# Kernel optimization log

Hardware: AMD Instinct MI355X
Metric: run time of the kernel (lower is better)

## Reference

```python
import jax, jax.numpy as jnp
import numpy as np

H, DQ, DK, DV, DM = 16, 64, 64, 64, 1024
NEG = -1.0e12


def setup_inputs() -> dict:
    key = jax.random.key(0)
    ks = jax.random.split(key, 16)
    B, S = 4, 1024
    s = 0.02
    inp = {
        "query": jax.random.normal(ks[0], (B, S, DM), jnp.float32),
        "key": jax.random.normal(ks[1], (B, S, DM), jnp.float32),
        "value": jax.random.normal(ks[2], (B, S, DM), jnp.float32),
        "mask": jax.random.randint(ks[3], (B, S), 0, 2, jnp.int32),
        "Wq": jax.random.normal(ks[4], (H * DQ, DM), jnp.float32) * s,
        "bq": jnp.zeros((H * DQ,), jnp.float32),
        "Wk": jax.random.normal(ks[5], (H * DK, DM), jnp.float32) * s,
        "bk": jnp.zeros((H * DK,), jnp.float32),
        "Wv": jax.random.normal(ks[6], (H * DV, DM), jnp.float32) * s,
        "bv": jnp.zeros((H * DV,), jnp.float32),
        "Wo": jax.random.normal(ks[7], (DM, H * DV), jnp.float32) * s,
        "bo": jnp.zeros((DM,), jnp.float32),
        "ln_g": jnp.ones((DM,), jnp.float32),
        "ln_b": jnp.zeros((DM,), jnp.float32),
    }
    return inp


def _attention(query, key, value, mask, Wq, bq, Wk, bk, Wv, bv, Wo, bo, ln_g, ln_b):
    B, qL, _ = query.shape
    kL = key.shape[1]
    mf = mask.astype(jnp.float32)  # [B, kL] ; 1 = masked token
    # padding mask broadcast over query rows, then self-attn: masked query rows fully masked
    m = jnp.broadcast_to(mf[:, None, :], (B, qL, kL))
    m = jnp.where(mf[:, :, None] > 0, 1.0, m)  # [B, q, k]

    def proj(x, W, b, d):
        # [B,S,DM] -> [H,B,S,d]
        return (x @ W.T + b).reshape(B, -1, H, d).transpose(2, 0, 1, 3)

    q = proj(query, Wq, bq, DQ)
    k = proj(key, Wk, bk, DK)
    v = proj(value, Wv, bv, DV)

    scores = jnp.einsum("hbqd,hbkd->hbqk", q, k) / np.float32(np.sqrt(DK))
    fut = jnp.triu(jnp.ones((qL, kL), jnp.float32), k=1)  # [q,k] future mask
    scores = scores + m[None] * NEG + fut[None, None] * NEG
    attn = jax.nn.softmax(scores, axis=-1)
    attn = attn * (1.0 - m[None]) * (1.0 - fut[None, None])

    out = jnp.einsum("hbqk,hbkd->hbqd", attn, v)  # [H,B,q,DV]
    out = out.transpose(1, 2, 0, 3).reshape(B, qL, H * DV)
    out = out @ Wo.T + bo + query  # residual
    mu = jnp.mean(out, axis=-1, keepdims=True)
    var = jnp.mean(jnp.square(out - mu), axis=-1, keepdims=True)
    out = (out - mu) * jax.lax.rsqrt(var + 1e-12) * ln_g + ln_b
    return out, attn.reshape(H * B, qL, kL)


def reference(query, key, value, mask, Wq, bq, Wk, bk, Wv, bv, Wo, bo, ln_g, ln_b):
    return _attention(query, key, value, mask, Wq, bq, Wk, bk, Wv, bv, Wo, bo, ln_g, ln_b)
```

## Files before the change

kernel.cpp:

```cpp
#include <hip/hip_runtime.h>
#include <hip/hip_bf16.h>

typedef __attribute__((ext_vector_type(4))) float f32x4;
typedef __attribute__((ext_vector_type(4))) float fv4;
typedef __attribute__((ext_vector_type(8))) short bf16x8;
typedef __attribute__((ext_vector_type(4))) short bf16x4;

#define DEVI __device__ __forceinline__

constexpr int BATCH = 4, SEQ = 1024, NH = 16, HD = 64, DM_ = 1024;
constexpr int NTOK = BATCH * SEQ;

DEVI unsigned short f2bf(float f) {
  union { float f; unsigned u; } v; v.f = f;
  unsigned r = v.u + 0x7FFFu + ((v.u >> 16) & 1u);
  return (unsigned short)(r >> 16);
}

DEVI int swz64(int row, int col) {
  int byte = (row * 64 + col) * 2;
  byte ^= (row & 7) << 4;
  return byte >> 1;
}

DEVI void gld_lds16(const unsigned short* g, unsigned short* l) {
  __builtin_amdgcn_global_load_lds(
      (const __attribute__((address_space(1))) unsigned int*)g,
      (__attribute__((address_space(3))) unsigned int*)l, 16, 0, 0);
}

__global__ __launch_bounds__(256) void k_cvt(
    const float* __restrict__ q, const float* __restrict__ k,
    const float* __restrict__ v,
    const float* __restrict__ wq, const float* __restrict__ wk,
    const float* __restrict__ wv, const float* __restrict__ wo,
    unsigned short* __restrict__ Xb, unsigned short* __restrict__ Wb)
{
  const int a = blockIdx.y;
  const float* src;
  unsigned short* dst;
  int n;
  if (a < 3) {
    src = (a == 0) ? q : (a == 1) ? k : v;
    dst = Xb + (size_t)a * NTOK * DM_;
    n = NTOK * DM_;
  } else {
    src = (a == 3) ? wq : (a == 4) ? wk : (a == 5) ? wv : wo;
    dst = Wb + (size_t)(a - 3) * DM_ * DM_;
    n = DM_ * DM_;
  }
  const int idx = (blockIdx.x * 256 + threadIdx.x) * 8;
  if (idx >= n) return;
  fv4 v0 = *(const fv4*)(src + idx);
  fv4 v1 = *(const fv4*)(src + idx + 4);
  bf16x8 o;
  o[0] = (short)f2bf(v0[0]); o[1] = (short)f2bf(v0[1]);
  o[2] = (short)f2bf(v0[2]); o[3] = (short)f2bf(v0[3]);
  o[4] = (short)f2bf(v1[0]); o[5] = (short)f2bf(v1[1]);
  o[6] = (short)f2bf(v1[2]); o[7] = (short)f2bf(v1[3]);
  *(bf16x8*)(dst + idx) = o;
}

__global__ __launch_bounds__(256) void k_proj(
    const unsigned short* __restrict__ Xb, const unsigned short* __restrict__ Wb,
    const float* __restrict__ bq, const float* __restrict__ bk,
    const float* __restrict__ bv,
    unsigned short* __restrict__ qo, unsigned short* __restrict__ ko,
    unsigned short* __restrict__ vTo)
{
  const int z = blockIdx.z;
  const unsigned short* X = Xb + (size_t)z * NTOK * DM_;
  const unsigned short* W = Wb + (size_t)z * DM_ * DM_;
  const float* bias = (z == 0) ? bq : (z == 1) ? bk : bv;

  __shared__ __align__(16) unsigned short Al[64 * 64];
  __shared__ __align__(16) unsigned short Bl[128 * 64];

  const int tid = threadIdx.x;
  const int lane = tid & 63;
  const int w = tid >> 6;
  const int wm = w & 1, wn = w >> 1;
  const int l15 = lane & 15, lg = lane >> 4;
  const int m0 = blockIdx.x * 64;
  const int o0 = blockIdx.y * 128;

  const int rseg = lane >> 3;
  const int cg = (lane & 7) ^ rseg;

  f32x4 acc[2][4];
#pragma unroll
  for (int i = 0; i < 2; ++i)
#pragma unroll
    for (int j = 0; j < 4; ++j) acc[i][j] = f32x4{0.f, 0.f, 0.f, 0.f};

  for (int kt = 0; kt < 16; ++kt) {
    const int k0 = kt * 64;
    __syncthreads();
#pragma unroll
    for (int i = 0; i < 2; ++i) {
      const int seg = w * 2 + i;
      gld_lds16(X + (size_t)(m0 + seg * 8 + rseg) * DM_ + k0 + cg * 8, &Al[seg * 512]);
    }
#pragma unroll
    for (int i = 0; i < 4; ++i) {
      const int seg = w * 4 + i;
      gld_lds16(W + (size_t)(o0 + seg * 8 + rseg) * DM_ + k0 + cg * 8, &Bl[seg * 512]);
    }
    __syncthreads();
#pragma unroll
    for (int kk = 0; kk < 2; ++kk) {
      bf16x8 af[2], bfm[4];
#pragma unroll
      for (int m = 0; m < 2; ++m)
        af[m] = *(const bf16x8*)&Al[swz64(wm * 32 + m * 16 + l15, kk * 32 + lg * 8)];
#pragma unroll
      for (int n = 0; n < 4; ++n)
        bfm[n] = *(const bf16x8*)&Bl[swz64(wn * 64 + n * 16 + l15, kk * 32 + lg * 8)];
#pragma unroll
      for (int m = 0; m < 2; ++m)
#pragma unroll
        for (int n = 0; n < 4; ++n)
          acc[m][n] = __builtin_amdgcn_mfma_f32_16x16x32_bf16(af[m], bfm[n], acc[m][n], 0, 0, 0);
    }
  }

#pragma unroll
  for (int n = 0; n < 4; ++n) {
    const int oc = o0 + wn * 64 + n * 16 + l15;
    const float bb = bias[oc];
#pragma unroll
    for (int m = 0; m < 2; ++m) {
      const int rbase = m0 + wm * 32 + m * 16 + lg * 4;
      if (z == 2) {
        bf16x4 pv;
#pragma unroll
        for (int j = 0; j < 4; ++j) pv[j] = (short)f2bf(acc[m][n][j] + bb);
        *(bf16x4*)&vTo[((size_t)(rbase >> 10) * 1024 + oc) * 1024 + (rbase & 1023)] = pv;
      } else {
        unsigned short* Y = (z == 0) ? qo : ko;
        const float sc = (z == 0) ? 0.125f : 1.f;
#pragma unroll
        for (int j = 0; j < 4; ++j)
          Y[(size_t)(rbase + j) * DM_ + oc] = f2bf((acc[m][n][j] + bb) * sc);
      }
    }
  }
}

__global__ __launch_bounds__(256) void k_attn_pv(
    const unsigned short* __restrict__ qb, const unsigned short* __restrict__ kb,
    const unsigned short* __restrict__ vT, const int* __restrict__ mask,
    float* __restrict__ attn, unsigned short* __restrict__ Ob)
{
  const int tid = threadIdx.x;
  const int lane = tid & 63;
  const int w = tid >> 6;
  const int l15 = lane & 15, lg = lane >> 4;
  const int hb = blockIdx.y;
  const int h = hb >> 2, b = hb & 3;
  const int t = blockIdx.x;
  const int q0 = t * 16;
  const int qglob = q0 + l15;

  __shared__ float Ow[4][64 * 18];
  __shared__ float red[4][16];
  __shared__ float ssum[16];

  const unsigned short* qp = qb + (size_t)(b * SEQ + qglob) * DM_ + h * HD + lg * 8;
  const bf16x8 qf0 = *(const bf16x8*)qp;
  const bf16x8 qf1 = *(const bf16x8*)(qp + 32);

  const int qm = mask[b * SEQ + qglob];
  const int ni = (t >= w) ? (((t - w) >> 2) + 1) : 0;

  f32x4 acc[16];
#pragma unroll
  for (int i = 0; i < 16; ++i) acc[i] = f32x4{0.f, 0.f, 0.f, 0.f};

#pragma unroll
  for (int i = 0; i < 16; ++i) {
    if (i < ni) {
      const int krow = (w + 4 * i) * 16 + l15;
      const unsigned short* kp = kb + (size_t)(b * SEQ + krow) * DM_ + h * HD + lg * 8;
      bf16x8 kf0 = *(const bf16x8*)kp;
      bf16x8 kf1 = *(const bf16x8*)(kp + 32);
      acc[i] = __builtin_amdgcn_mfma_f32_16x16x32_bf16(kf0, qf0, acc[i], 0, 0, 0);
      acc[i] = __builtin_amdgcn_mfma_f32_16x16x32_bf16(kf1, qf1, acc[i], 0, 0, 0);
    }
  }

  unsigned long long kv = 0;
#pragma unroll
  for (int i = 0; i < 16; ++i) {
    if (i < ni) {
      const int kbase = (w + 4 * i) * 16 + lg * 4;
      int4 mv = *(const int4*)&mask[b * SEQ + kbase];
      if (mv.x == 0) kv |= 1ull << (i * 4 + 0);
      if (mv.y == 0) kv |= 1ull << (i * 4 + 1);
      if (mv.z == 0) kv |= 1ull << (i * 4 + 2);
      if (mv.w == 0) kv |= 1ull << (i * 4 + 3);
    }
  }
  if (qm != 0) kv = 0;

  float m = -1e30f;
#pragma unroll
  for (int i = 0; i < 16; ++i) {
    if (i < ni) {
      const int kbase = (w + 4 * i) * 16 + lg * 4;
#pragma unroll
      for (int j = 0; j < 4; ++j)
        if (((kv >> (i * 4 + j)) & 1ull) && (kbase + j <= qglob))
          m = fmaxf(m, acc[i][j]);
    }
  }
  m = fmaxf(m, __shfl_xor(m, 16, 64));
  m = fmaxf(m, __shfl_xor(m, 32, 64));
  if (lane < 16) red[w][l15] = m;
  __syncthreads();
  m = fmaxf(fmaxf(red[0][l15], red[1][l15]), fmaxf(red[2][l15], red[3][l15]));
  __syncthreads();

  float s = 0.f;
#pragma unroll
  for (int i = 0; i < 16; ++i) {
    if (i < ni) {
      const int kbase = (w + 4 * i) * 16 + lg * 4;
#pragma unroll
      for (int j = 0; j < 4; ++j) {
        const bool vld = ((kv >> (i * 4 + j)) & 1ull) && (kbase + j <= qglob);
        const float p = vld ? __expf(acc[i][j] - m) : 0.f;
        acc[i][j] = p;
        s += p;
      }
    }
  }
  s += __shfl_xor(s, 16, 64);
  s += __shfl_xor(s, 32, 64);
  if (lane < 16) red[w][l15] = s;
  __syncthreads();
  s = red[0][l15] + red[1][l15] + red[2][l15] + red[3][l15];
  if (w == 0 && lane < 16) ssum[l15] = s;
  const float rinv = (s > 0.f) ? (1.f / s) : 0.f;

  float* ap = attn + (size_t)hb * SEQ * SEQ + (size_t)qglob * SEQ;
#pragma unroll
  for (int i = 0; i < 16; ++i) {
    const int kbase = (w + 4 * i) * 16 + lg * 4;
    fv4 st = fv4{0.f, 0.f, 0.f, 0.f};
    if (i < ni) {
#pragma unroll
      for (int j = 0; j < 4; ++j) st[j] = acc[i][j] * rinv;
    }
    *(fv4*)&ap[kbase] = st;
  }

  f32x4 o[4];
#pragma unroll
  for (int dt = 0; dt < 4; ++dt) o[dt] = f32x4{0.f, 0.f, 0.f, 0.f};
  const int nc = (ni + 1) >> 1;
  const unsigned short* vbase = vT + (size_t)(b * 1024 + h * HD) * 1024;
#pragma unroll
  for (int c = 0; c < 8; ++c) {
    if (c < nc) {
      const bool hasB = (2 * c + 1 < ni);
      bf16x8 pb;
#pragma unroll
      for (int j = 0; j < 4; ++j) pb[j] = (short)f2bf(acc[2 * c][j]);
#pragma unroll
      for (int j = 0; j < 4; ++j)
        pb[4 + j] = hasB ? (short)f2bf(acc[2 * c + 1][j]) : (short)0;
      const int kA = (w + 8 * c) * 16 + lg * 4;
      const int kB = hasB ? kA + 64 : kA;
#pragma unroll
      for (int dt = 0; dt < 4; ++dt) {
        const unsigned short* vr = vbase + (size_t)(dt * 16 + l15) * 1024;
        bf16x4 a0 = *(const bf16x4*)(vr + kA);
        bf16x4 a1 = *(const bf16x4*)(vr + kB);
        bf16x8 af;
        af[0] = a0[0]; af[1] = a0[1]; af[2] = a0[2]; af[3] = a0[3];
        af[4] = a1[0]; af[5] = a1[1]; af[6] = a1[2]; af[7] = a1[3];
        o[dt] = __builtin_amdgcn_mfma_f32_16x16x32_bf16(af, pb, o[dt], 0, 0, 0);
      }
    }
  }

#pragma unroll
  for (int dt = 0; dt < 4; ++dt)
#pragma unroll
    for (int j = 0; j < 4; ++j)
      Ow[w][(dt * 16 + lg * 4 + j) * 18 + l15] = o[dt][j];
  __syncthreads();

  const int qr = tid >> 4;
  const int d0 = (tid & 15) * 4;
  const float sq = ssum[qr];
  const float ri = (sq > 0.f) ? (1.f / sq) : 0.f;
  bf16x4 ob;
#pragma unroll
  for (int j = 0; j < 4; ++j) {
    const int d = d0 + j;
    const float v = Ow[0][d * 18 + qr] + Ow[1][d * 18 + qr] +
                    Ow[2][d * 18 + qr] + Ow[3][d * 18 + qr];
    ob[j] = (short)f2bf(v * ri);
  }
  *(bf16x4*)&Ob[(size_t)(b * SEQ + q0 + qr) * DM_ + h * HD + d0] = ob;
}

__global__ __launch_bounds__(256) void k_oproj(
    const unsigned short* __restrict__ Ob, const unsigned short* __restrict__ Wb,
    const float* __restrict__ bo, const float* __restrict__ query,
    float* __restrict__ preln)
{
  const unsigned short* W = Wb + (size_t)3 * DM_ * DM_;

  __shared__ __align__(16) unsigned short Al[64 * 64];
  __shared__ __align__(16) unsigned short Bl[128 * 64];

  const int tid = threadIdx.x;
  const int lane = tid & 63;
  const int w = tid >> 6;
  const int wm = w & 1, wn = w >> 1;
  const int l15 = lane & 15, lg = lane >> 4;
  const int m0 = blockIdx.x * 64;
  const int o0 = blockIdx.y * 128;

  const int rseg = lane >> 3;
  const int cg = (lane & 7) ^ rseg;

  f32x4 acc[2][4];
#pragma unroll
  for (int i = 0; i < 2; ++i)
#pragma unroll
    for (int j = 0; j < 4; ++j) acc[i][j] = f32x4{0.f, 0.f, 0.f, 0.f};

  for (int kt = 0; kt < 16; ++kt) {
    const int k0 = kt * 64;
    __syncthreads();
#pragma unroll
    for (int i = 0; i < 2; ++i) {
      const int seg = w * 2 + i;
      gld_lds16(Ob + (size_t)(m0 + seg * 8 + rseg) * DM_ + k0 + cg * 8, &Al[seg * 512]);
    }
#pragma unroll
    for (int i = 0; i < 4; ++i) {
      const int seg = w * 4 + i;
      gld_lds16(W + (size_t)(o0 + seg * 8 + rseg) * DM_ + k0 + cg * 8, &Bl[seg * 512]);
    }
    __syncthreads();
#pragma unroll
    for (int kk = 0; kk < 2; ++kk) {
      bf16x8 af[2], bfm[4];
#pragma unroll
      for (int m = 0; m < 2; ++m)
        af[m] = *(const bf16x8*)&Al[swz64(wm * 32 + m * 16 + l15, kk * 32 + lg * 8)];
#pragma unroll
      for (int n = 0; n < 4; ++n)
        bfm[n] = *(const bf16x8*)&Bl[swz64(wn * 64 + n * 16 + l15, kk * 32 + lg * 8)];
#pragma unroll
      for (int m = 0; m < 2; ++m)
#pragma unroll
        for (int n = 0; n < 4; ++n)
          acc[m][n] = __builtin_amdgcn_mfma_f32_16x16x32_bf16(af[m], bfm[n], acc[m][n], 0, 0, 0);
    }
  }

#pragma unroll
  for (int n = 0; n < 4; ++n) {
    const int oc = o0 + wn * 64 + n * 16 + l15;
    const float bb = bo[oc];
#pragma unroll
    for (int m = 0; m < 2; ++m) {
      const int rbase = m0 + wm * 32 + m * 16 + lg * 4;
#pragma unroll
      for (int j = 0; j < 4; ++j) {
        const size_t idx = (size_t)(rbase + j) * DM_ + oc;
        preln[idx] = acc[m][n][j] + bb + query[idx];
      }
    }
  }
}

__global__ __launch_bounds__(256) void k_ln(
    const float* __restrict__ x, const float* __restrict__ g,
    const float* __restrict__ bta, float* __restrict__ out)
{
  const int row = blockIdx.x;
  const int tid = threadIdx.x;
  const float* xr = x + (size_t)row * DM_;
  fv4 v = *(const fv4*)(xr + tid * 4);
  float s = v[0] + v[1] + v[2] + v[3];
  float s2 = v[0] * v[0] + v[1] * v[1] + v[2] * v[2] + v[3] * v[3];
#pragma unroll
  for (int off = 1; off < 64; off <<= 1) {
    s += __shfl_xor(s, off, 64);
    s2 += __shfl_xor(s2, off, 64);
  }
  __shared__ float rs[2][4];
  const int w = tid >> 6;
  if ((tid & 63) == 0) { rs[0][w] = s; rs[1][w] = s2; }
  __syncthreads();
  s = rs[0][0] + rs[0][1] + rs[0][2] + rs[0][3];
  s2 = rs[1][0] + rs[1][1] + rs[1][2] + rs[1][3];
  const float mu = s * (1.f / 1024.f);
  const float var = s2 * (1.f / 1024.f) - mu * mu;
  const float rstd = rsqrtf(var + 1e-12f);
  fv4 gg = *(const fv4*)(g + tid * 4);
  fv4 bb = *(const fv4*)(bta + tid * 4);
  fv4 o;
#pragma unroll
  for (int j = 0; j < 4; ++j) o[j] = (v[j] - mu) * rstd * gg[j] + bb[j];
  *(fv4*)(out + (size_t)row * DM_ + tid * 4) = o;
}

extern "C" void kernel_launch(void* const* d_in, const int* in_sizes, int n_in,
                              void* d_out, int out_size, void* d_ws, size_t ws_size,
                              hipStream_t stream) {
  const float* query = (const float*)d_in[0];
  const float* key   = (const float*)d_in[1];
  const float* value = (const float*)d_in[2];
  const int*   mask  = (const int*)d_in[3];
  const float* Wq = (const float*)d_in[4];
  const float* bq = (const float*)d_in[5];
  const float* Wk = (const float*)d_in[6];
  const float* bk = (const float*)d_in[7];
  const float* Wv = (const float*)d_in[8];
  const float* bv = (const float*)d_in[9];
  const float* Wo = (const float*)d_in[10];
  const float* bo = (const float*)d_in[11];
  const float* ln_g = (const float*)d_in[12];
  const float* ln_b = (const float*)d_in[13];

  float* out  = (float*)d_out;
  float* attn = out + (size_t)NTOK * DM_;

  char* ws = (char*)d_ws;
  unsigned short* Xb = (unsigned short*)ws;
  unsigned short* Wb = Xb + (size_t)3 * NTOK * DM_;
  unsigned short* qb = Wb + (size_t)4 * DM_ * DM_;
  unsigned short* kb = qb + (size_t)NTOK * DM_;
  unsigned short* vT = kb + (size_t)NTOK * DM_;
  unsigned short* Ob = vT + (size_t)NTOK * DM_;
  float* preln = (float*)ws;

  k_cvt<<<dim3(2048, 7), 256, 0, stream>>>(query, key, value, Wq, Wk, Wv, Wo,
                                           Xb, Wb);
  k_proj<<<dim3(64, 8, 3), 256, 0, stream>>>(Xb, Wb, bq, bk, bv, qb, kb, vT);
  k_attn_pv<<<dim3(64, 64), 256, 0, stream>>>(qb, kb, vT, mask, attn, Ob);
  k_oproj<<<dim3(64, 8), 256, 0, stream>>>(Ob, Wb, bo, query, preln);
  k_ln<<<4096, 256, 0, stream>>>(preln, ln_g, ln_b, out);
}
```

Baseline: 557.3 us.

## Double-buffer projection GEMMs and restructure attention to 32-query blocks with LDS P tile

The q/k/v and output projection GEMMs switch to two LDS buffers, so the next k-tile's global-to-LDS load is issued while MFMAs run on the current tile. This drops one barrier per iteration in exchange for twice the shared memory. The attention kernel now uses 512-thread blocks covering 32 queries, so each K fragment is reused across two query groups. Probabilities are staged in a swizzled LDS tile, so the PV product reads contiguous V rows split across two k-halves. The larger LDS footprint (64KB for P) and higher register use may reduce occupancy.

```diff
diff --git a/kernel.cpp b/kernel.cpp
--- a/kernel.cpp
+++ b/kernel.cpp
@@ -73,8 +73,8 @@
   const unsigned short* W = Wb + (size_t)z * DM_ * DM_;
   const float* bias = (z == 0) ? bq : (z == 1) ? bk : bv;
 
-  __shared__ __align__(16) unsigned short Al[64 * 64];
-  __shared__ __align__(16) unsigned short Bl[128 * 64];
+  __shared__ __align__(16) unsigned short Al[2][64 * 64];
+  __shared__ __align__(16) unsigned short Bl[2][128 * 64];
 
   const int tid = threadIdx.x;
   const int lane = tid & 63;
@@ -93,35 +93,43 @@
 #pragma unroll
     for (int j = 0; j < 4; ++j) acc[i][j] = f32x4{0.f, 0.f, 0.f, 0.f};
 
+#define PROJ_STAGE(nb, kt)                                                     \
+  {                                                                            \
+    const int k0_ = (kt) * 64;                                                 \
+    _Pragma("unroll") for (int i = 0; i < 2; ++i) {                            \
+      const int seg = w * 2 + i;                                               \
+      gld_lds16(X + (size_t)(m0 + seg * 8 + rseg) * DM_ + k0_ + cg * 8,        \
+                &Al[nb][seg * 512]);                                           \
+    }                                                                          \
+    _Pragma("unroll") for (int i = 0; i < 4; ++i) {                            \
+      const int seg = w * 4 + i;                                               \
+      gld_lds16(W + (size_t)(o0 + seg * 8 + rseg) * DM_ + k0_ + cg * 8,        \
+                &Bl[nb][seg * 512]);                                           \
+    }                                                                          \
+  }
+
+  PROJ_STAGE(0, 0);
+  __syncthreads();
+
   for (int kt = 0; kt < 16; ++kt) {
-    const int k0 = kt * 64;
-    __syncthreads();
-#pragma unroll
-    for (int i = 0; i < 2; ++i) {
-      const int seg = w * 2 + i;
-      gld_lds16(X + (size_t)(m0 + seg * 8 + rseg) * DM_ + k0 + cg * 8, &Al[seg * 512]);
-    }
-#pragma unroll
-    for (int i = 0; i < 4; ++i) {
-      const int seg = w * 4 + i;
-      gld_lds16(W + (size_t)(o0 + seg * 8 + rseg) * DM_ + k0 + cg * 8, &Bl[seg * 512]);
-    }
-    __syncthreads();
+    const int cur = kt & 1;
+    if (kt < 15) PROJ_STAGE(cur ^ 1, kt + 1);
 #pragma unroll
     for (int kk = 0; kk < 2; ++kk) {
       bf16x8 af[2], bfm[4];
 #pragma unroll
       for (int m = 0; m < 2; ++m)
-        af[m] = *(const bf16x8*)&Al[swz64(wm * 32 + m * 16 + l15, kk * 32 + lg * 8)];
+        af[m] = *(const bf16x8*)&Al[cur][swz64(wm * 32 + m * 16 + l15, kk * 32 + lg * 8)];
 #pragma unroll
       for (int n = 0; n < 4; ++n)
-        bfm[n] = *(const bf16x8*)&Bl[swz64(wn * 64 + n * 16 + l15, kk * 32 + lg * 8)];
+        bfm[n] = *(const bf16x8*)&Bl[cur][swz64(wn * 64 + n * 16 + l15, kk * 32 + lg * 8)];
 #pragma unroll
       for (int m = 0; m < 2; ++m)
 #pragma unroll
         for (int n = 0; n < 4; ++n)
           acc[m][n] = __builtin_amdgcn_mfma_f32_16x16x32_bf16(af[m], bfm[n], acc[m][n], 0, 0, 0);
     }
+    __syncthreads();
   }
 
 #pragma unroll
@@ -147,7 +155,7 @@
   }
 }
 
-__global__ __launch_bounds__(256) void k_attn_pv(
+__global__ __launch_bounds__(512, 2) void k_attn_pv(
     const unsigned short* __restrict__ qb, const unsigned short* __restrict__ kb,
     const unsigned short* __restrict__ vT, const int* __restrict__ mask,
     float* __restrict__ attn, unsigned short* __restrict__ Ob)
@@ -158,153 +166,207 @@
   const int l15 = lane & 15, lg = lane >> 4;
   const int hb = blockIdx.y;
   const int h = hb >> 2, b = hb & 3;
-  const int t = blockIdx.x;
-  const int q0 = t * 16;
-  const int qglob = q0 + l15;
-
-  __shared__ float Ow[4][64 * 18];
-  __shared__ float red[4][16];
-  __shared__ float ssum[16];
-
-  const unsigned short* qp = qb + (size_t)(b * SEQ + qglob) * DM_ + h * HD + lg * 8;
-  const bf16x8 qf0 = *(const bf16x8*)qp;
-  const bf16x8 qf1 = *(const bf16x8*)(qp + 32);
-
-  const int qm = mask[b * SEQ + qglob];
-  const int ni = (t >= w) ? (((t - w) >> 2) + 1) : 0;
-
-  f32x4 acc[16];
-#pragma unroll
-  for (int i = 0; i < 16; ++i) acc[i] = f32x4{0.f, 0.f, 0.f, 0.f};
-
-#pragma unroll
-  for (int i = 0; i < 16; ++i) {
+  const int bx = blockIdx.x;
+  const int q0 = bx * 32;
+
+  __shared__ __align__(16) unsigned short Pl[32 * 1024];
+  __shared__ float red[8][2][16];
+  __shared__ float ssum[32];
+
+  int qglob[2];
+  qglob[0] = q0 + l15;
+  qglob[1] = q0 + 16 + l15;
+
+  bf16x8 qf[2][2];
+#pragma unroll
+  for (int g = 0; g < 2; ++g) {
+    const unsigned short* qp = qb + (size_t)(b * SEQ + qglob[g]) * DM_ + h * HD + lg * 8;
+    qf[g][0] = *(const bf16x8*)qp;
+    qf[g][1] = *(const bf16x8*)(qp + 32);
+  }
+  int qm[2];
+  qm[0] = mask[b * SEQ + qglob[0]];
+  qm[1] = mask[b * SEQ + qglob[1]];
+
+  const int tt = 2 * bx + 1;
+  const int ni = (tt >= w) ? ((tt - w) >> 3) + 1 : 0;
+
+  bf16x8 kf[8][2];
+#pragma unroll
+  for (int i = 0; i < 8; ++i) {
     if (i < ni) {
-      const int krow = (w + 4 * i) * 16 + l15;
+      const int krow = (w + 8 * i) * 16 + l15;
       const unsigned short* kp = kb + (size_t)(b * SEQ + krow) * DM_ + h * HD + lg * 8;
-      bf16x8 kf0 = *(const bf16x8*)kp;
-      bf16x8 kf1 = *(const bf16x8*)(kp + 32);
-      acc[i] = __builtin_amdgcn_mfma_f32_16x16x32_bf16(kf0, qf0, acc[i], 0, 0, 0);
-      acc[i] = __builtin_amdgcn_mfma_f32_16x16x32_bf16(kf1, qf1, acc[i], 0, 0, 0);
-    }
-  }
-
-  unsigned long long kv = 0;
-#pragma unroll
-  for (int i = 0; i < 16; ++i) {
+      kf[i][0] = *(const bf16x8*)kp;
+      kf[i][1] = *(const bf16x8*)(kp + 32);
+    }
+  }
+
+  f32x4 acc[8][2];
+#pragma unroll
+  for (int i = 0; i < 8; ++i)
+#pragma unroll
+    for (int g = 0; g < 2; ++g) acc[i][g] = f32x4{0.f, 0.f, 0.f, 0.f};
+
+#pragma unroll
+  for (int i = 0; i < 8; ++i) {
     if (i < ni) {
-      const int kbase = (w + 4 * i) * 16 + lg * 4;
+#pragma unroll
+      for (int g = 0; g < 2; ++g) {
+        acc[i][g] = __builtin_amdgcn_mfma_f32_16x16x32_bf16(kf[i][0], qf[g][0], acc[i][g], 0, 0, 0);
+        acc[i][g] = __builtin_amdgcn_mfma_f32_16x16x32_bf16(kf[i][1], qf[g][1], acc[i][g], 0, 0, 0);
+      }
+    }
+  }
+
+  unsigned kvb = 0;
+#pragma unroll
+  for (int i = 0; i < 8; ++i) {
+    if (i < ni) {
+      const int kbase = (w + 8 * i) * 16 + lg * 4;
       int4 mv = *(const int4*)&mask[b * SEQ + kbase];
-      if (mv.x == 0) kv |= 1ull << (i * 4 + 0);
-      if (mv.y == 0) kv |= 1ull << (i * 4 + 1);
-      if (mv.z == 0) kv |= 1ull << (i * 4 + 2);
-      if (mv.w == 0) kv |= 1ull << (i * 4 + 3);
-    }
-  }
-  if (qm != 0) kv = 0;
-
-  float m = -1e30f;
-#pragma unroll
-  for (int i = 0; i < 16; ++i) {
+      if (mv.x == 0) kvb |= 1u << (i * 4 + 0);
+      if (mv.y == 0) kvb |= 1u << (i * 4 + 1);
+      if (mv.z == 0) kvb |= 1u << (i * 4 + 2);
+      if (mv.w == 0) kvb |= 1u << (i * 4 + 3);
+    }
+  }
+
+  float m[2] = {-1e30f, -1e30f};
+#pragma unroll
+  for (int i = 0; i < 8; ++i) {
     if (i < ni) {
-      const int kbase = (w + 4 * i) * 16 + lg * 4;
-#pragma unroll
-      for (int j = 0; j < 4; ++j)
-        if (((kv >> (i * 4 + j)) & 1ull) && (kbase + j <= qglob))
-          m = fmaxf(m, acc[i][j]);
-    }
-  }
-  m = fmaxf(m, __shfl_xor(m, 16, 64));
-  m = fmaxf(m, __shfl_xor(m, 32, 64));
-  if (lane < 16) red[w][l15] = m;
-  __syncthreads();
-  m = fmaxf(fmaxf(red[0][l15], red[1][l15]), fmaxf(red[2][l15], red[3][l15]));
-  __syncthreads();
-
-  float s = 0.f;
-#pragma unroll
-  for (int i = 0; i < 16; ++i) {
+      const int kbase = (w + 8 * i) * 16 + lg * 4;
+#pragma unroll
+      for (int j = 0; j < 4; ++j) {
+        if ((kvb >> (i * 4 + j)) & 1u) {
+#pragma unroll
+          for (int g = 0; g < 2; ++g)
+            if (qm[g] == 0 && kbase + j <= qglob[g]) m[g] = fmaxf(m[g], acc[i][g][j]);
+        }
+      }
+    }
+  }
+#pragma unroll
+  for (int g = 0; g < 2; ++g) {
+    m[g] = fmaxf(m[g], __shfl_xor(m[g], 16, 64));
+    m[g] = fmaxf(m[g], __shfl_xor(m[g], 32, 64));
+  }
+  if (lane < 16) { red[w][0][l15] = m[0]; red[w][1][l15] = m[1]; }
+  __syncthreads();
+#pragma unroll
+  for (int g = 0; g < 2; ++g) {
+    float mm = red[0][g][l15];
+#pragma unroll
+    for (int ww = 1; ww < 8; ++ww) mm = fmaxf(mm, red[ww][g][l15]);
+    m[g] = mm;
+  }
+  __syncthreads();
+
+  float s[2] = {0.f, 0.f};
+#pragma unroll
+  for (int i = 0; i < 8; ++i) {
     if (i < ni) {
-      const int kbase = (w + 4 * i) * 16 + lg * 4;
+      const int kbase = (w + 8 * i) * 16 + lg * 4;
 #pragma unroll
       for (int j = 0; j < 4; ++j) {
-        const bool vld = ((kv >> (i * 4 + j)) & 1ull) && (kbase + j <= qglob);
-        const float p = vld ? __expf(acc[i][j] - m) : 0.f;
-        acc[i][j] = p;
-        s += p;
-      }
-    }
-  }
-  s += __shfl_xor(s, 16, 64);
-  s += __shfl_xor(s, 32, 64);
-  if (lane < 16) red[w][l15] = s;
-  __syncthreads();
-  s = red[0][l15] + red[1][l15] + red[2][l15] + red[3][l15];
-  if (w == 0 && lane < 16) ssum[l15] = s;
-  const float rinv = (s > 0.f) ? (1.f / s) : 0.f;
-
-  float* ap = attn + (size_t)hb * SEQ * SEQ + (size_t)qglob * SEQ;
-#pragma unroll
-  for (int i = 0; i < 16; ++i) {
-    const int kbase = (w + 4 * i) * 16 + lg * 4;
-    fv4 st = fv4{0.f, 0.f, 0.f, 0.f};
-    if (i < ni) {
-#pragma unroll
-      for (int j = 0; j < 4; ++j) st[j] = acc[i][j] * rinv;
-    }
-    *(fv4*)&ap[kbase] = st;
-  }
-
-  f32x4 o[4];
-#pragma unroll
-  for (int dt = 0; dt < 4; ++dt) o[dt] = f32x4{0.f, 0.f, 0.f, 0.f};
-  const int nc = (ni + 1) >> 1;
-  const unsigned short* vbase = vT + (size_t)(b * 1024 + h * HD) * 1024;
-#pragma unroll
-  for (int c = 0; c < 8; ++c) {
-    if (c < nc) {
-      const bool hasB = (2 * c + 1 < ni);
-      bf16x8 pb;
-#pragma unroll
-      for (int j = 0; j < 4; ++j) pb[j] = (short)f2bf(acc[2 * c][j]);
-#pragma unroll
-      for (int j = 0; j < 4; ++j)
-        pb[4 + j] = hasB ? (short)f2bf(acc[2 * c + 1][j]) : (short)0;
-      const int kA = (w + 8 * c) * 16 + lg * 4;
-      const int kB = hasB ? kA + 64 : kA;
-#pragma unroll
-      for (int dt = 0; dt < 4; ++dt) {
-        const unsigned short* vr = vbase + (size_t)(dt * 16 + l15) * 1024;
-        bf16x4 a0 = *(const bf16x4*)(vr + kA);
-        bf16x4 a1 = *(const bf16x4*)(vr + kB);
-        bf16x8 af;
-        af[0] = a0[0]; af[1] = a0[1]; af[2] = a0[2]; af[3] = a0[3];
-        af[4] = a1[0]; af[5] = a1[1]; af[6] = a1[2]; af[7] = a1[3];
-        o[dt] = __builtin_amdgcn_mfma_f32_16x16x32_bf16(af, pb, o[dt], 0, 0, 0);
-      }
-    }
-  }
-
-#pragma unroll
-  for (int dt = 0; dt < 4; ++dt)
-#pragma unroll
-    for (int j = 0; j < 4; ++j)
-      Ow[w][(dt * 16 + lg * 4 + j) * 18 + l15] = o[dt][j];
-  __syncthreads();
-
-  const int qr = tid >> 4;
+        const bool kok = (kvb >> (i * 4 + j)) & 1u;
+#pragma unroll
+        for (int g = 0; g < 2; ++g) {
+          const bool vld = kok && (qm[g] == 0) && (kbase + j <= qglob[g]);
+          const float p = vld ? __expf(acc[i][g][j] - m[g]) : 0.f;
+          acc[i][g][j] = p;
+          s[g] += p;
+        }
+      }
+    }
+  }
+#pragma unroll
+  for (int g = 0; g < 2; ++g) {
+    s[g] += __shfl_xor(s[g], 16, 64);
+    s[g] += __shfl_xor(s[g], 32, 64);
+  }
+  if (lane < 16) { red[w][0][l15] = s[0]; red[w][1][l15] = s[1]; }
+  __syncthreads();
+  float rinv[2];
+#pragma unroll
+  for (int g = 0; g < 2; ++g) {
+    float sm = 0.f;
+#pragma unroll
+    for (int ww = 0; ww < 8; ++ww) sm += red[ww][g][l15];
+    s[g] = sm;
+    rinv[g] = (sm > 0.f) ? (1.f / sm) : 0.f;
+  }
+  if (w == 0 && lane < 16) { ssum[l15] = s[0]; ssum[16 + l15] = s[1]; }
+
+#pragma unroll
+  for (int i = 0; i < 8; ++i) {
+    const int kbase = (w + 8 * i) * 16 + lg * 4;
+#pragma unroll
+    for (int g = 0; g < 2; ++g) {
+      float* ap = attn + (size_t)hb * SEQ * SEQ + (size_t)qglob[g] * SEQ;
+      fv4 st = fv4{0.f, 0.f, 0.f, 0.f};
+      bf16x4 pb = bf16x4{0, 0, 0, 0};
+      if (i < ni) {
+#pragma unroll
+        for (int j = 0; j < 4; ++j) {
+          st[j] = acc[i][g][j] * rinv[g];
+          pb[j] = (short)f2bf(acc[i][g][j]);
+        }
+      }
+      *(fv4*)&ap[kbase] = st;
+      const int row = g * 16 + l15;
+      const int pbyte = ((row * 1024 + kbase) * 2) ^ ((l15 & 7) << 4);
+      *(bf16x4*)((char*)Pl + pbyte) = pb;
+    }
+  }
+  __syncthreads();
+
+  const int dt = w & 3, kh = w >> 2;
+  f32x4 o[2];
+  o[0] = f32x4{0.f, 0.f, 0.f, 0.f};
+  o[1] = f32x4{0.f, 0.f, 0.f, 0.f};
+  const unsigned short* vr = vT + (size_t)(b * 1024 + h * HD + dt * 16 + l15) * 1024;
+#pragma unroll 4
+  for (int j = 0; j < 16; ++j) {
+    const int kt = 2 * j + kh;
+    if (kt <= bx) {
+      const int k0 = kt * 32 + lg * 8;
+      bf16x8 vf = *(const bf16x8*)(vr + k0);
+#pragma unroll
+      for (int g = 0; g < 2; ++g) {
+        const int row = g * 16 + l15;
+        const int pbyte = ((row * 1024 + k0) * 2) ^ ((l15 & 7) << 4);
+        bf16x8 pf = *(const bf16x8*)((const char*)Pl + pbyte);
+        o[g] = __builtin_amdgcn_mfma_f32_16x16x32_bf16(vf, pf, o[g], 0, 0, 0);
+      }
+    }
+  }
+  __syncthreads();
+
+  float* Ow = (float*)Pl;
+#pragma unroll
+  for (int g = 0; g < 2; ++g) {
+    const int qloc = g * 16 + l15;
+#pragma unroll
+    for (int j = 0; j < 4; ++j) {
+      const int d = dt * 16 + lg * 4 + j;
+      Ow[(kh * 64 + d) * 33 + qloc] = o[g][j];
+    }
+  }
+  __syncthreads();
+
+  const int qloc = tid >> 4;
   const int d0 = (tid & 15) * 4;
-  const float sq = ssum[qr];
+  const float sq = ssum[qloc];
   const float ri = (sq > 0.f) ? (1.f / sq) : 0.f;
   bf16x4 ob;
 #pragma unroll
   for (int j = 0; j < 4; ++j) {
-    const int d = d0 + j;
-    const float v = Ow[0][d * 18 + qr] + Ow[1][d * 18 + qr] +
-                    Ow[2][d * 18 + qr] + Ow[3][d * 18 + qr];
+    const float v = Ow[(0 * 64 + d0 + j) * 33 + qloc] + Ow[(1 * 64 + d0 + j) * 33 + qloc];
     ob[j] = (short)f2bf(v * ri);
   }
-  *(bf16x4*)&Ob[(size_t)(b * SEQ + q0 + qr) * DM_ + h * HD + d0] = ob;
+  *(bf16x4*)&Ob[(size_t)(b * SEQ + q0 + qloc) * DM_ + h * HD + d0] = ob;
 }
 
 __global__ __launch_bounds__(256) void k_oproj(
@@ -314,8 +376,8 @@
 {
   const unsigned short* W = Wb + (size_t)3 * DM_ * DM_;
 
-  __shared__ __align__(16) unsigned short Al[64 * 64];
-  __shared__ __align__(16) unsigned short Bl[128 * 64];
+  __shared__ __align__(16) unsigned short Al[2][64 * 64];
+  __shared__ __align__(16) unsigned short Bl[2][128 * 64];
 
   const int tid = threadIdx.x;
   const int lane = tid & 63;
@@ -334,35 +396,43 @@
 #pragma unroll
     for (int j = 0; j < 4; ++j) acc[i][j] = f32x4{0.f, 0.f, 0.f, 0.f};
 
+#define OPROJ_STAGE(nb, kt)                                                    \
+  {                                                                            \
+    const int k0_ = (kt) * 64;                                                 \
+    _Pragma("unroll") for (int i = 0; i < 2; ++i) {                            \
+      const int seg = w * 2 + i;                                               \
+      gld_lds16(Ob + (size_t)(m0 + seg * 8 + rseg) * DM_ + k0_ + cg * 8,       \
+                &Al[nb][seg * 512]);                                           \
+    }                                                                          \
+    _Pragma("unroll") for (int i = 0; i < 4; ++i) {                            \
+      const int seg = w * 4 + i;                                               \
+      gld_lds16(W + (size_t)(o0 + seg * 8 + rseg) * DM_ + k0_ + cg * 8,        \
+                &Bl[nb][seg * 512]);                                           \
+    }                                                                          \
+  }
+
+  OPROJ_STAGE(0, 0);
+  __syncthreads();
+
   for (int kt = 0; kt < 16; ++kt) {
-    const int k0 = kt * 64;
-    __syncthreads();
-#pragma unroll
-    for (int i = 0; i < 2; ++i) {
-      const int seg = w * 2 + i;
-      gld_lds16(Ob + (size_t)(m0 + seg * 8 + rseg) * DM_ + k0 + cg * 8, &Al[seg * 512]);
-    }
-#pragma unroll
-    for (int i = 0; i < 4; ++i) {
-      const int seg = w * 4 + i;
-      gld_lds16(W + (size_t)(o0 + seg * 8 + rseg) * DM_ + k0 + cg * 8, &Bl[seg * 512]);
-    }
-    __syncthreads();
+    const int cur = kt & 1;
+    if (kt < 15) OPROJ_STAGE(cur ^ 1, kt + 1);
 #pragma unroll
     for (int kk = 0; kk < 2; ++kk) {
       bf16x8 af[2], bfm[4];
 #pragma unroll
       for (int m = 0; m < 2; ++m)
-        af[m] = *(const bf16x8*)&Al[swz64(wm * 32 + m * 16 + l15, kk * 32 + lg * 8)];
+        af[m] = *(const bf16x8*)&Al[cur][swz64(wm * 32 + m * 16 + l15, kk * 32 + lg * 8)];
 #pragma unroll
       for (int n = 0; n < 4; ++n)
-        bfm[n] = *(const bf16x8*)&Bl[swz64(wn * 64 + n * 16 + l15, kk * 32 + lg * 8)];
+        bfm[n] = *(const bf16x8*)&Bl[cur][swz64(wn * 64 + n * 16 + l15, kk * 32 + lg * 8)];
 #pragma unroll
       for (int m = 0; m < 2; ++m)
 #pragma unroll
         for (int n = 0; n < 4; ++n)
           acc[m][n] = __builtin_amdgcn_mfma_f32_16x16x32_bf16(af[m], bfm[n], acc[m][n], 0, 0, 0);
     }
+    __syncthreads();
   }
 
 #pragma unroll
@@ -446,7 +516,7 @@
   k_cvt<<<dim3(2048, 7), 256, 0, stream>>>(query, key, value, Wq, Wk, Wv, Wo,
                                            Xb, Wb);
   k_proj<<<dim3(64, 8, 3), 256, 0, stream>>>(Xb, Wb, bq, bk, bv, qb, kb, vT);
-  k_attn_pv<<<dim3(64, 64), 256, 0, stream>>>(qb, kb, vT, mask, attn, Ob);
+  k_attn_pv<<<dim3(32, 64), 512, 0, stream>>>(qb, kb, vT, mask, attn, Ob);
   k_oproj<<<dim3(64, 8), 256, 0, stream>>>(Ob, Wb, bo, query, preln);
   k_ln<<<4096, 256, 0, stream>>>(preln, ln_g, ln_b, out);
 }
```

Result: faster. 504.9 us (-9.4%).
